# Optimization experiments

Measured on AMD Instinct MI355X. Metric: run time of the kernel, lower is better.

The kernel has to match this reference:

```python
import jax, jax.numpy as jnp
import numpy as np

B, S, D = 4, 4096, 1024
P = int(D * 1.333)  # 1364, matches torch int(d_model * proj_factor)
CAP = 15.0
EPS = 1e-6


def _rmsnorm(x, w, eps=EPS):
    xf = x.astype(jnp.float32)
    var = jnp.mean(xf * xf, axis=-1, keepdims=True)
    return w * (xf * jax.lax.rsqrt(var + eps)).astype(x.dtype)


def _softcap_sigmoid(g):
    # sigmoid(cap * tanh(g / cap))
    return jax.nn.sigmoid(CAP * jnp.tanh(g / CAP))


def setup_inputs() -> dict:
    key = jax.random.key(0)
    k0, k1, k2, k3 = jax.random.split(key, 4)
    x = jax.random.normal(k0, (B, S, D), jnp.float32)
    hidden_state = jnp.zeros((B, P), jnp.float32)
    ln_weight = jnp.ones((D,), jnp.float32)
    W_gate = jax.random.normal(k1, (D, 3 * P), jnp.float32) / np.sqrt(D).astype(np.float32)
    W_cell = jax.random.normal(k2, (D, P), jnp.float32) / np.sqrt(D).astype(np.float32)
    W_out = jax.random.normal(k3, (P, D), jnp.float32) / np.sqrt(P).astype(np.float32)
    return {"x": x, "hidden_state": hidden_state, "ln_weight": ln_weight,
            "W_gate": W_gate, "W_cell": W_cell, "W_out": W_out}


def reference(x, hidden_state, ln_weight, W_gate, W_cell, W_out):
    b, s, d = x.shape
    residual = x
    xn = _rmsnorm(x, ln_weight)
    # gate projection -> [b, s, 3, P], unbind gate types
    gates = jnp.einsum('bsd,dk->bsk', xn, W_gate).reshape(b, s, 3, P)
    i_gate = _softcap_sigmoid(gates[:, :, 0])
    f_gate = _softcap_sigmoid(gates[:, :, 1])
    o_gate = _softcap_sigmoid(gates[:, :, 2])
    c_input = jnp.einsum('bsd,dp->bsp', xn, W_cell)

    # sequential linear recurrence: h_t = f_t * h_{t-1} + i_t * tanh(c_t)
    def step(h, inp):
        c_t, i_t, f_t, o_t = inp
        h = f_t * h + i_t * jnp.tanh(c_t)
        return h, o_t * jnp.tanh(h)

    seq = (jnp.swapaxes(c_input, 0, 1), jnp.swapaxes(i_gate, 0, 1),
           jnp.swapaxes(f_gate, 0, 1), jnp.swapaxes(o_gate, 0, 1))  # time-major [s,b,P]
    _, outs = jax.lax.scan(step, hidden_state, seq)
    outputs = jnp.swapaxes(outs, 0, 1)  # [b, s, P]

    out = residual + jnp.einsum('bsp,pd->bsd', outputs, W_out)
    # NOTE: original torch module returns the UNMODIFIED initial hidden_state
    return out, hidden_state
```

## Files before the change

### kernel.cpp

```cpp
#include <hip/hip_runtime.h>
#include <hip/hip_bf16.h>
#include <math.h>
#include <stdint.h>

typedef __bf16 bf16_t;
typedef bf16_t bf16x4 __attribute__((ext_vector_type(4)));
typedef bf16_t bf16x8 __attribute__((ext_vector_type(8)));
typedef float floatx4 __attribute__((ext_vector_type(4)));

#define B_     4
#define S_     4096
#define D_     1024
#define P_     1364
#define P3_    4092
#define NP_    5456
#define NPAD_  5504
#define NB_    5632
#define KPAD_  1408
#define ROWS_  16384
#define CAP_   15.0f
#define EPS_   1e-6f
#define CHUNKS_ 32
#define CLEN_   128

__device__ __forceinline__ float fast_tanh(float x) {
    x = fminf(fmaxf(x, -15.f), 15.f);
    float e = __expf(2.f * x);
    return __fdividef(e - 1.f, e + 1.f);
}
__device__ __forceinline__ float fast_softcap_sig(float g) {
    float t = fast_tanh(g * (1.0f / CAP_));
    return __fdividef(1.f, 1.f + __expf(-CAP_ * t));
}

template <int N>
__device__ __forceinline__ void vmcnt_wait() {
    if constexpr (N == 8)      asm volatile("s_waitcnt vmcnt(8)" ::: "memory");
    else if constexpr (N == 4) asm volatile("s_waitcnt vmcnt(4)" ::: "memory");
    else if constexpr (N == 0) asm volatile("s_waitcnt vmcnt(0)" ::: "memory");
}

__global__ __launch_bounds__(256) void rmsnorm_kernel(const float* __restrict__ x,
                                                      const float* __restrict__ w,
                                                      bf16_t* __restrict__ xn) {
    int row = blockIdx.x;
    int tid = threadIdx.x;
    const float4 v = ((const float4*)(x + (size_t)row * D_))[tid];
    float ss = v.x * v.x + v.y * v.y + v.z * v.z + v.w * v.w;
    #pragma unroll
    for (int off = 32; off > 0; off >>= 1) ss += __shfl_down(ss, off);
    __shared__ float red[4];
    if ((tid & 63) == 0) red[tid >> 6] = ss;
    __syncthreads();
    float tot = red[0] + red[1] + red[2] + red[3];
    float scale = rsqrtf(tot * (1.0f / (float)D_) + EPS_);
    const float4 wv = ((const float4*)w)[tid];
    bf16x4 o;
    o[0] = (bf16_t)(v.x * scale * wv.x);
    o[1] = (bf16_t)(v.y * scale * wv.y);
    o[2] = (bf16_t)(v.z * scale * wv.z);
    o[3] = (bf16_t)(v.w * scale * wv.w);
    ((bf16x4*)(xn + (size_t)row * D_))[tid] = o;
}

__global__ __launch_bounds__(256) void pack_wcat(const float* __restrict__ Wg,
                                                 const float* __restrict__ Wc,
                                                 bf16_t* __restrict__ Wt) {
    __shared__ float tile[32][33];
    int kt = blockIdx.x * 32;
    int nt = blockIdx.y * 32;
    int tx = threadIdx.x & 31;
    int ty = threadIdx.x >> 5;
    #pragma unroll
    for (int i = 0; i < 4; i++) {
        int k = kt + ty + 8 * i;
        int n = nt + tx;
        float val = 0.f;
        if (n < P3_)      val = Wg[(size_t)k * P3_ + n];
        else if (n < NP_) val = Wc[(size_t)k * P_ + (n - P3_)];
        tile[ty + 8 * i][tx] = val;
    }
    __syncthreads();
    #pragma unroll
    for (int i = 0; i < 4; i++) {
        int n = nt + ty + 8 * i;
        int k = kt + tx;
        Wt[(size_t)n * D_ + k] = (bf16_t)tile[tx][ty + 8 * i];
    }
}

__global__ __launch_bounds__(256) void pack_wout(const float* __restrict__ Wo,
                                                 bf16_t* __restrict__ Wt) {
    __shared__ float tile[32][33];
    int pt = blockIdx.x * 32;
    int dt = blockIdx.y * 32;
    int tx = threadIdx.x & 31;
    int ty = threadIdx.x >> 5;
    #pragma unroll
    for (int i = 0; i < 4; i++) {
        int p = pt + ty + 8 * i;
        int d = dt + tx;
        float val = (p < P_) ? Wo[(size_t)p * D_ + d] : 0.f;
        tile[ty + 8 * i][tx] = val;
    }
    __syncthreads();
    #pragma unroll
    for (int i = 0; i < 4; i++) {
        int d = dt + ty + 8 * i;
        int p = pt + tx;
        Wt[(size_t)d * KPAD_ + p] = (bf16_t)tile[tx][ty + 8 * i];
    }
}


#define PH_SYNC                                                               \
    __builtin_amdgcn_s_barrier();                                             \
    asm volatile("s_waitcnt lgkmcnt(0)" ::: "memory");                        \
    __builtin_amdgcn_sched_barrier(0);

#define MFMA_ROW(NLO)                                                         \
    _Pragma("unroll")                                                         \
    for (int m = 0; m < 8; m++) {                                             \
      acc[m][NLO]     = __builtin_amdgcn_mfma_f32_16x16x32_bf16(af[m], b0, acc[m][NLO], 0, 0, 0);     \
      acc[m][NLO + 1] = __builtin_amdgcn_mfma_f32_16x16x32_bf16(af[m], b1, acc[m][NLO + 1], 0, 0, 0); \
    }

#define K_ITER(KT, CB, DO_NXT, DO_CUR, VMA, VMB)                              \
  {                                                                           \
    _Pragma("unroll") for (int m = 0; m < 8; m++) af[m] = ldA(CB, 0, m);      \
    b0 = ldB(CB, 0, 0); b1 = ldB(CB, 0, 1);                                   \
    if (DO_NXT) stA((KT) + 1, 1, (CB) ^ 1);                                   \
    PH_SYNC                                                                   \
    __builtin_amdgcn_s_setprio(1);                                            \
    MFMA_ROW(0)                                                               \
    __builtin_amdgcn_s_setprio(0);                                            \
    __builtin_amdgcn_s_barrier();                                             \
    b0 = ldB(CB, 0, 2); b1 = ldB(CB, 0, 3);                                   \
    if (DO_NXT) stB((KT) + 1, 1, (CB) ^ 1);                                   \
    PH_SYNC                                                                   \
    __builtin_amdgcn_s_setprio(1);                                            \
    MFMA_ROW(2)                                                               \
    __builtin_amdgcn_s_setprio(0);                                            \
    vmcnt_wait<VMA>();                                                        \
    __builtin_amdgcn_s_barrier();                                             \
    _Pragma("unroll") for (int m = 0; m < 8; m++) af[m] = ldA(CB, 1, m);      \
    b0 = ldB(CB, 1, 0); b1 = ldB(CB, 1, 1);                                   \
    if (DO_CUR) stA((KT) + 2, 0, (CB));                                       \
    PH_SYNC                                                                   \
    __builtin_amdgcn_s_setprio(1);                                            \
    MFMA_ROW(0)                                                               \
    __builtin_amdgcn_s_setprio(0);                                            \
    __builtin_amdgcn_s_barrier();                                             \
    b0 = ldB(CB, 1, 2); b1 = ldB(CB, 1, 3);                                   \
    if (DO_CUR) stB((KT) + 2, 0, (CB));                                       \
    PH_SYNC                                                                   \
    __builtin_amdgcn_s_setprio(1);                                            \
    MFMA_ROW(2)                                                               \
    __builtin_amdgcn_s_setprio(0);                                            \
    vmcnt_wait<VMB>();                                                        \
    __builtin_amdgcn_s_barrier();                                             \
  }

template <int KTOT, int LDA, int LDB, int LDC, int NX, int EPI>
__global__ __launch_bounds__(512, 2) void gemm8(const bf16_t* __restrict__ A,
                                                const bf16_t* __restrict__ Bt,
                                                const float* __restrict__ res,
                                                void* __restrict__ outv) {
    constexpr int NT = KTOT / 64;
    static_assert(NT % 2 == 0 && NT >= 4, "NT must be even, >=4");
    __shared__ __align__(16) char smem[131072];

    const int tid  = threadIdx.x;
    const int wid  = tid >> 6;
    const int lane = tid & 63;
    const int l15  = lane & 15;
    const int sl4  = lane >> 4;
    const int sp    = sl4 ^ ((lane >> 1) & 3);
    const int chunk = (lane & 3) ^ ((lane >> 3) & 3);
    const int wrow = (wid >> 2) * 128;
    const int wcol = (wid & 3) * 64;

    constexpr int NWG = NX * (ROWS_ / 256);
    constexpr int CPX = NWG / 8;
    int lin = blockIdx.x;
    lin = (lin & 7) * CPX + (lin >> 3);
    const int by = lin / NX, bx = lin % NX;
    const int m0 = by * 256, n0 = bx * 256;

    const int srow = wid * 16 + (lane >> 2);
    const bf16_t* Asrc = A  + (size_t)(m0 + srow) * LDA + chunk * 8;
    const bf16_t* Bsrc = Bt + (size_t)(n0 + srow) * LDB + chunk * 8;
    const unsigned ldsA0 = (unsigned)(wid * 1024);
    const unsigned ldsB0 = 32768u + (unsigned)(wid * 1024);

    auto stA = [&](int kt, int kk, int buf) {
        const bf16_t* s = Asrc + kt * 64 + kk * 32;
        char* d = smem + ((unsigned)buf * 65536u + (unsigned)kk * 16384u + ldsA0);
        __builtin_amdgcn_global_load_lds((const unsigned*)s, (unsigned*)d, 16, 0, 0);
        __builtin_amdgcn_global_load_lds((const unsigned*)(s + (size_t)128 * LDA),
                                         (unsigned*)(d + 8192), 16, 0, 0);
    };
    auto stB = [&](int kt, int kk, int buf) {
        const bf16_t* s = Bsrc + kt * 64 + kk * 32;
        char* d = smem + ((unsigned)buf * 65536u + (unsigned)kk * 16384u + ldsB0);
        __builtin_amdgcn_global_load_lds((const unsigned*)s, (unsigned*)d, 16, 0, 0);
        __builtin_amdgcn_global_load_lds((const unsigned*)(s + (size_t)128 * LDB),
                                         (unsigned*)(d + 8192), 16, 0, 0);
    };
    auto ldA = [&](int buf, int kk, int m) -> bf16x8 {
        return *(const bf16x8*)(smem + (buf * 65536 + kk * 16384 +
                                        (wrow + m * 16 + l15) * 64 + sp * 16));
    };
    auto ldB = [&](int buf, int kk, int n) -> bf16x8 {
        return *(const bf16x8*)(smem + (buf * 65536 + 32768 + kk * 16384 +
                                        (wcol + n * 16 + l15) * 64 + sp * 16));
    };

    floatx4 acc[8][4];
    #pragma unroll
    for (int m = 0; m < 8; m++)
        #pragma unroll
        for (int n = 0; n < 4; n++) acc[m][n] = (floatx4){0.f, 0.f, 0.f, 0.f};
    bf16x8 af[8], b0, b1;

    stA(0, 0, 0); stB(0, 0, 0);
    stA(0, 1, 0); stB(0, 1, 0);
    stA(1, 0, 1); stB(1, 0, 1);
    vmcnt_wait<8>();
    __builtin_amdgcn_s_barrier();

    for (int kt = 0; kt < NT - 2; kt += 2) {
        K_ITER(kt,     0, true, true, 8, 8)
        K_ITER(kt + 1, 1, true, true, 8, 8)
    }
    K_ITER(NT - 2, 0, true,  false, 8, 4)
    K_ITER(NT - 1, 1, false, false, 0, -1)

    const int crow = m0 + wrow + sl4 * 4;
    const int ccol = n0 + wcol + l15;
    if constexpr (EPI == 0) {
        bf16_t* O = (bf16_t*)outv;
        #pragma unroll
        for (int m = 0; m < 8; m++)
            #pragma unroll
            for (int n = 0; n < 4; n++) {
                const int col = ccol + n * 16;
                if (col < NPAD_) {
                    #pragma unroll
                    for (int r = 0; r < 4; r++) {
                        const int row = crow + m * 16 + r;
                        float g = acc[m][n][r];
                        float v = (col < P3_) ? fast_softcap_sig(g) : fast_tanh(g);
                        O[(size_t)row * LDC + col] = (bf16_t)v;
                    }
                }
            }
    } else {
        float* O = (float*)outv;
        #pragma unroll
        for (int m = 0; m < 8; m++)
            #pragma unroll
            for (int n = 0; n < 4; n++) {
                const int col = ccol + n * 16;
                #pragma unroll
                for (int r = 0; r < 4; r++) {
                    const int row = crow + m * 16 + r;
                    O[(size_t)row * LDC + col] = res[(size_t)row * LDC + col] + acc[m][n][r];
                }
            }
    }
}

__global__ __launch_bounds__(256) void chunk_scan1(const bf16_t* __restrict__ act,
                                                   float* __restrict__ FA) {
    int p = blockIdx.x * 256 + threadIdx.x;
    int c = blockIdx.y;
    int b = blockIdx.z;
    if (p >= P_) return;
    const bf16_t* base = act + (size_t)(b * S_ + c * CLEN_) * NPAD_;
    float F = 1.f, Acc = 0.f;
    for (int t = 0; t < CLEN_; t++) {
        const bf16_t* r = base + (size_t)t * NPAD_;
        float iv = (float)r[p];
        float fv = (float)r[P_ + p];
        float tc = (float)r[P3_ + p];
        Acc = fv * Acc + iv * tc;
        F *= fv;
    }
    size_t idx = (((size_t)b * CHUNKS_ + c) * P_ + p) * 2;
    FA[idx]     = F;
    FA[idx + 1] = Acc;
}

__global__ __launch_bounds__(256) void chunk_scan2(const bf16_t* __restrict__ act,
                                                   const float* __restrict__ FA,
                                                   const float* __restrict__ h0,
                                                   bf16_t* __restrict__ outp) {
    int p = blockIdx.x * 256 + threadIdx.x;
    int c = blockIdx.y;
    int b = blockIdx.z;
    if (p >= KPAD_) return;
    if (p >= P_) {
        bf16_t z = (bf16_t)0.f;
        for (int t = 0; t < CLEN_; t++)
            outp[(size_t)(b * S_ + c * CLEN_ + t) * KPAD_ + p] = z;
        return;
    }
    float h = h0[(size_t)b * P_ + p];
    for (int j = 0; j < c; j++) {
        size_t idx = (((size_t)b * CHUNKS_ + j) * P_ + p) * 2;
        h = FA[idx + 1] + FA[idx] * h;
    }
    const bf16_t* base = act + (size_t)(b * S_ + c * CLEN_) * NPAD_;
    bf16_t* ob = outp + (size_t)(b * S_ + c * CLEN_) * KPAD_;
    for (int t = 0; t < CLEN_; t++) {
        const bf16_t* r = base + (size_t)t * NPAD_;
        float iv = (float)r[p];
        float fv = (float)r[P_ + p];
        float ov = (float)r[2 * P_ + p];
        float tc = (float)r[P3_ + p];
        h = fv * h + iv * tc;
        ob[(size_t)t * KPAD_ + p] = (bf16_t)(ov * fast_tanh(h));
    }
}

__global__ void copy_hidden(const float* __restrict__ hs, float* __restrict__ dst) {
    int i = blockIdx.x * 256 + threadIdx.x;
    if (i < B_ * P_) dst[i] = hs[i];
}

extern "C" void kernel_launch(void* const* d_in, const int* in_sizes, int n_in,
                              void* d_out, int out_size, void* d_ws, size_t ws_size,
                              hipStream_t stream) {
    const float* x   = (const float*)d_in[0];
    const float* hs  = (const float*)d_in[1];
    const float* lnw = (const float*)d_in[2];
    const float* Wg  = (const float*)d_in[3];
    const float* Wc  = (const float*)d_in[4];
    const float* Wo  = (const float*)d_in[5];
    float* out = (float*)d_out;

    char* ws = (char*)d_ws;
    size_t off = 0;
    auto alloc = [&](size_t bytes) {
        void* p = ws + off;
        off += (bytes + 255) & ~(size_t)255;
        return p;
    };
    bf16_t* xn_outp = (bf16_t*)alloc((size_t)ROWS_ * KPAD_ * 2);
    bf16_t* act     = (bf16_t*)alloc((size_t)ROWS_ * NPAD_ * 2);
    bf16_t* WcatT   = (bf16_t*)alloc((size_t)NB_ * D_ * 2);
    bf16_t* WoutT   = (bf16_t*)alloc((size_t)D_ * KPAD_ * 2);
    float*  FA      = (float*)alloc((size_t)B_ * CHUNKS_ * P_ * 2 * 4);

    bf16_t* xn   = xn_outp;
    bf16_t* outp = xn_outp;

    hipLaunchKernelGGL(rmsnorm_kernel, dim3(ROWS_), dim3(256), 0, stream, x, lnw, xn);
    hipLaunchKernelGGL(pack_wcat, dim3(32, NB_ / 32), dim3(256), 0, stream, Wg, Wc, WcatT);
    hipLaunchKernelGGL(pack_wout, dim3(KPAD_ / 32, D_ / 32), dim3(256), 0, stream, Wo, WoutT);

    hipLaunchKernelGGL((gemm8<D_, D_, D_, NPAD_, NB_ / 256, 0>),
                       dim3((NB_ / 256) * (ROWS_ / 256)), dim3(512), 0, stream,
                       xn, WcatT, (const float*)nullptr, (void*)act);

    hipLaunchKernelGGL(chunk_scan1, dim3(6, CHUNKS_, B_), dim3(256), 0, stream, act, FA);
    hipLaunchKernelGGL(chunk_scan2, dim3(6, CHUNKS_, B_), dim3(256), 0, stream, act, FA, hs, outp);

    hipLaunchKernelGGL((gemm8<KPAD_, KPAD_, KPAD_, D_, D_ / 256, 1>),
                       dim3((D_ / 256) * (ROWS_ / 256)), dim3(512), 0, stream,
                       outp, WoutT, x, d_out);

    hipLaunchKernelGGL(copy_hidden, dim3((B_ * P_ + 255) / 256), dim3(256), 0, stream,
                       hs, out + (size_t)ROWS_ * D_);
}
```

Baseline: 467.0 us.

## Replace interleaved ping-pong GEMM pipeline with simple double-buffered loop and XCD-major tile mapping

Drops the hand-interleaved K_ITER schedule, which split each K-tile into four phases with barriers and staged loads between MFMA groups. It is replaced by a plain loop: load all A/B fragments for both k-halves, issue 64 MFMAs, then stage tile t+2 into the freed buffer behind two barriers. The workgroup-to-tile mapping also changes so each XCD owns a contiguous band of M rows and walks N tiles, aiming for better L2 reuse of A. The risk is less overlap between global loads, LDS reads and MFMAs, plus higher register pressure from holding 24 fragment vectors at once.

```diff
diff --git a/kernel.cpp b/kernel.cpp
--- a/kernel.cpp
+++ b/kernel.cpp
@@ -36,7 +36,6 @@
 template <int N>
 __device__ __forceinline__ void vmcnt_wait() {
     if constexpr (N == 8)      asm volatile("s_waitcnt vmcnt(8)" ::: "memory");
-    else if constexpr (N == 4) asm volatile("s_waitcnt vmcnt(4)" ::: "memory");
     else if constexpr (N == 0) asm volatile("s_waitcnt vmcnt(0)" ::: "memory");
 }
 
@@ -112,62 +111,13 @@
     }
 }
 
-
-#define PH_SYNC                                                               \
-    __builtin_amdgcn_s_barrier();                                             \
-    asm volatile("s_waitcnt lgkmcnt(0)" ::: "memory");                        \
-    __builtin_amdgcn_sched_barrier(0);
-
-#define MFMA_ROW(NLO)                                                         \
-    _Pragma("unroll")                                                         \
-    for (int m = 0; m < 8; m++) {                                             \
-      acc[m][NLO]     = __builtin_amdgcn_mfma_f32_16x16x32_bf16(af[m], b0, acc[m][NLO], 0, 0, 0);     \
-      acc[m][NLO + 1] = __builtin_amdgcn_mfma_f32_16x16x32_bf16(af[m], b1, acc[m][NLO + 1], 0, 0, 0); \
-    }
-
-#define K_ITER(KT, CB, DO_NXT, DO_CUR, VMA, VMB)                              \
-  {                                                                           \
-    _Pragma("unroll") for (int m = 0; m < 8; m++) af[m] = ldA(CB, 0, m);      \
-    b0 = ldB(CB, 0, 0); b1 = ldB(CB, 0, 1);                                   \
-    if (DO_NXT) stA((KT) + 1, 1, (CB) ^ 1);                                   \
-    PH_SYNC                                                                   \
-    __builtin_amdgcn_s_setprio(1);                                            \
-    MFMA_ROW(0)                                                               \
-    __builtin_amdgcn_s_setprio(0);                                            \
-    __builtin_amdgcn_s_barrier();                                             \
-    b0 = ldB(CB, 0, 2); b1 = ldB(CB, 0, 3);                                   \
-    if (DO_NXT) stB((KT) + 1, 1, (CB) ^ 1);                                   \
-    PH_SYNC                                                                   \
-    __builtin_amdgcn_s_setprio(1);                                            \
-    MFMA_ROW(2)                                                               \
-    __builtin_amdgcn_s_setprio(0);                                            \
-    vmcnt_wait<VMA>();                                                        \
-    __builtin_amdgcn_s_barrier();                                             \
-    _Pragma("unroll") for (int m = 0; m < 8; m++) af[m] = ldA(CB, 1, m);      \
-    b0 = ldB(CB, 1, 0); b1 = ldB(CB, 1, 1);                                   \
-    if (DO_CUR) stA((KT) + 2, 0, (CB));                                       \
-    PH_SYNC                                                                   \
-    __builtin_amdgcn_s_setprio(1);                                            \
-    MFMA_ROW(0)                                                               \
-    __builtin_amdgcn_s_setprio(0);                                            \
-    __builtin_amdgcn_s_barrier();                                             \
-    b0 = ldB(CB, 1, 2); b1 = ldB(CB, 1, 3);                                   \
-    if (DO_CUR) stB((KT) + 2, 0, (CB));                                       \
-    PH_SYNC                                                                   \
-    __builtin_amdgcn_s_setprio(1);                                            \
-    MFMA_ROW(2)                                                               \
-    __builtin_amdgcn_s_setprio(0);                                            \
-    vmcnt_wait<VMB>();                                                        \
-    __builtin_amdgcn_s_barrier();                                             \
-  }
-
 template <int KTOT, int LDA, int LDB, int LDC, int NX, int EPI>
 __global__ __launch_bounds__(512, 2) void gemm8(const bf16_t* __restrict__ A,
                                                 const bf16_t* __restrict__ Bt,
                                                 const float* __restrict__ res,
                                                 void* __restrict__ outv) {
     constexpr int NT = KTOT / 64;
-    static_assert(NT % 2 == 0 && NT >= 4, "NT must be even, >=4");
+    static_assert(NT >= 4, "NT >= 4");
     __shared__ __align__(16) char smem[131072];
 
     const int tid  = threadIdx.x;
@@ -180,11 +130,12 @@
     const int wrow = (wid >> 2) * 128;
     const int wcol = (wid & 3) * 64;
 
-    constexpr int NWG = NX * (ROWS_ / 256);
-    constexpr int CPX = NWG / 8;
-    int lin = blockIdx.x;
-    lin = (lin & 7) * CPX + (lin >> 3);
-    const int by = lin / NX, bx = lin % NX;
+    constexpr int MCH = (ROWS_ / 256) / 8;
+    const int bid = blockIdx.x;
+    const int xcd = bid & 7;
+    const int idx = bid >> 3;
+    const int bx  = idx / MCH;
+    const int by  = xcd * MCH + (idx - bx * MCH);
     const int m0 = by * 256, n0 = bx * 256;
 
     const int srow = wid * 16 + (lane >> 2);
@@ -193,19 +144,20 @@
     const unsigned ldsA0 = (unsigned)(wid * 1024);
     const unsigned ldsB0 = 32768u + (unsigned)(wid * 1024);
 
-    auto stA = [&](int kt, int kk, int buf) {
-        const bf16_t* s = Asrc + kt * 64 + kk * 32;
-        char* d = smem + ((unsigned)buf * 65536u + (unsigned)kk * 16384u + ldsA0);
-        __builtin_amdgcn_global_load_lds((const unsigned*)s, (unsigned*)d, 16, 0, 0);
-        __builtin_amdgcn_global_load_lds((const unsigned*)(s + (size_t)128 * LDA),
-                                         (unsigned*)(d + 8192), 16, 0, 0);
-    };
-    auto stB = [&](int kt, int kk, int buf) {
-        const bf16_t* s = Bsrc + kt * 64 + kk * 32;
-        char* d = smem + ((unsigned)buf * 65536u + (unsigned)kk * 16384u + ldsB0);
-        __builtin_amdgcn_global_load_lds((const unsigned*)s, (unsigned*)d, 16, 0, 0);
-        __builtin_amdgcn_global_load_lds((const unsigned*)(s + (size_t)128 * LDB),
-                                         (unsigned*)(d + 8192), 16, 0, 0);
+    auto stage = [&](int kt, int buf) {
+        #pragma unroll
+        for (int kk = 0; kk < 2; kk++) {
+            const bf16_t* sa = Asrc + kt * 64 + kk * 32;
+            char* da = smem + ((unsigned)buf * 65536u + (unsigned)kk * 16384u + ldsA0);
+            __builtin_amdgcn_global_load_lds((const unsigned*)sa, (unsigned*)da, 16, 0, 0);
+            __builtin_amdgcn_global_load_lds((const unsigned*)(sa + (size_t)128 * LDA),
+                                             (unsigned*)(da + 8192), 16, 0, 0);
+            const bf16_t* sb = Bsrc + kt * 64 + kk * 32;
+            char* db = smem + ((unsigned)buf * 65536u + (unsigned)kk * 16384u + ldsB0);
+            __builtin_amdgcn_global_load_lds((const unsigned*)sb, (unsigned*)db, 16, 0, 0);
+            __builtin_amdgcn_global_load_lds((const unsigned*)(sb + (size_t)128 * LDB),
+                                             (unsigned*)(db + 8192), 16, 0, 0);
+        }
     };
     auto ldA = [&](int buf, int kk, int m) -> bf16x8 {
         return *(const bf16x8*)(smem + (buf * 65536 + kk * 16384 +
@@ -221,20 +173,47 @@
     for (int m = 0; m < 8; m++)
         #pragma unroll
         for (int n = 0; n < 4; n++) acc[m][n] = (floatx4){0.f, 0.f, 0.f, 0.f};
-    bf16x8 af[8], b0, b1;
-
-    stA(0, 0, 0); stB(0, 0, 0);
-    stA(0, 1, 0); stB(0, 1, 0);
-    stA(1, 0, 1); stB(1, 0, 1);
+
+    bf16x8 a0[8], b0v[4], a1[8], b1v[4];
+
+    stage(0, 0);
+    stage(1, 1);
     vmcnt_wait<8>();
     __builtin_amdgcn_s_barrier();
 
-    for (int kt = 0; kt < NT - 2; kt += 2) {
-        K_ITER(kt,     0, true, true, 8, 8)
-        K_ITER(kt + 1, 1, true, true, 8, 8)
-    }
-    K_ITER(NT - 2, 0, true,  false, 8, 4)
-    K_ITER(NT - 1, 1, false, false, 0, -1)
+    for (int t = 0; t < NT; ++t) {
+        const int c = t & 1;
+        #pragma unroll
+        for (int m = 0; m < 8; m++) a0[m] = ldA(c, 0, m);
+        #pragma unroll
+        for (int n = 0; n < 4; n++) b0v[n] = ldB(c, 0, n);
+        #pragma unroll
+        for (int m = 0; m < 8; m++) a1[m] = ldA(c, 1, m);
+        #pragma unroll
+        for (int n = 0; n < 4; n++) b1v[n] = ldB(c, 1, n);
+
+        __builtin_amdgcn_s_setprio(1);
+        #pragma unroll
+        for (int m = 0; m < 8; m++)
+            #pragma unroll
+            for (int n = 0; n < 4; n++)
+                acc[m][n] = __builtin_amdgcn_mfma_f32_16x16x32_bf16(a0[m], b0v[n], acc[m][n], 0, 0, 0);
+        #pragma unroll
+        for (int m = 0; m < 8; m++)
+            #pragma unroll
+            for (int n = 0; n < 4; n++)
+                acc[m][n] = __builtin_amdgcn_mfma_f32_16x16x32_bf16(a1[m], b1v[n], acc[m][n], 0, 0, 0);
+        __builtin_amdgcn_s_setprio(0);
+
+        __builtin_amdgcn_s_barrier();
+        if (t + 2 < NT) {
+            stage(t + 2, c);
+            vmcnt_wait<8>();
+        } else if (t + 2 == NT) {
+            vmcnt_wait<0>();
+        }
+        __builtin_amdgcn_s_barrier();
+    }
 
     const int crow = m0 + wrow + sl4 * 4;
     const int ccol = n0 + wcol + l15;
```

Result: slower. 501.6 us (+7.4%).
